# Optimization experiments

Measured on AMD Instinct MI355X. Metric: run time of the kernel, lower is better.

## Reference

```python
import jax, jax.numpy as jnp
import numpy as np

N, E, G, H = 100000, 1600000, 256, 2
EPS = 1e-5


def _gat_conv(x, src, dst, W, a_src, a_dst, bias, C):
    # PyG GATConv (concat=True, negative_slope=0.2): lin has no bias, bias added after concat.
    h = (x @ W).reshape(N, H, C)                                   # [N,H,C]
    e_src = (h * a_src).sum(-1)                                    # [N,H]
    e_dst = (h * a_dst).sum(-1)                                    # [N,H]
    alpha = jax.nn.leaky_relu(e_src[src] + e_dst[dst], 0.2)        # [Etot,H]
    amax = jax.ops.segment_max(alpha, dst, num_segments=N)         # segment softmax over incoming edges
    ex = jnp.exp(alpha - amax[dst])
    denom = jax.ops.segment_sum(ex, dst, num_segments=N)
    msg = h[src] * ex[:, :, None]                                  # [Etot,H,C]
    out = jax.ops.segment_sum(msg, dst, num_segments=N) / (denom[:, :, None] + 1e-16)
    return out.reshape(N, H * C) + bias


def _bn(x, g, b, m, v):  # BatchNorm in eval mode with running stats
    return g * (x - m) * jax.lax.rsqrt(v + EPS) + b


def _forward(edge_index, batch, x, w1, as1, ad1, b1, g1, be1, m1, v1, p1w, p1b,
             w2, as2, ad2, b2, g2, be2, m2, v2, p2w, p2b,
             w3, as3, ad3, b3, g3, be3, m3, v3, p3w, p3b,
             fw, fb, g4, be4, m4, v4, l1w, l1b, l2w, l2b):
    loops = jnp.arange(N, dtype=edge_index.dtype)                  # GATConv add_self_loops=True
    src = jnp.concatenate([edge_index[0], loops])
    dst = jnp.concatenate([edge_index[1], loops])
    h = jax.nn.relu(_bn(_gat_conv(x, src, dst, w1, as1, ad1, b1, 32), g1, be1, m1, v1)) + (x @ p1w + p1b)
    h = jax.nn.relu(_bn(_gat_conv(h, src, dst, w2, as2, ad2, b2, 64), g2, be2, m2, v2)) + (h @ p2w + p2b)
    h = jax.nn.relu(_bn(_gat_conv(h, src, dst, w3, as3, ad3, b3, 64), g3, be3, m3, v3)) + (h @ p3w + p3b)
    counts = jax.ops.segment_sum(jnp.ones((N,), h.dtype), batch, num_segments=G)
    pooled = jax.ops.segment_sum(h, batch, num_segments=G) / jnp.maximum(counts, 1.0)[:, None]  # [G,128]
    z = jax.nn.relu(_bn(pooled @ fw + fb, g4, be4, m4, v4))
    z = jax.nn.relu(z @ l1w + l1b)
    return z @ l2w + l2b                                           # [G,10]


def setup_inputs():
    key = jax.random.key(0)
    ks = jax.random.split(key, 48)
    it = iter(range(48))
    def rn(shape, s=0.1):
        return jax.random.normal(ks[next(it)], shape, jnp.float32) * s
    def bn_params(dim):  # gamma, beta, running_mean, running_var
        return (jax.random.uniform(ks[next(it)], (dim,), jnp.float32, 0.5, 1.5),
                rn((dim,)), rn((dim,)),
                jax.random.uniform(ks[next(it)], (dim,), jnp.float32, 0.5, 1.5))
    inp = {}
    inp["x"] = jax.random.normal(ks[next(it)], (N, 5), jnp.float32)
    inp["edge_index"] = jax.random.randint(ks[next(it)], (2, E), 0, N, jnp.int32)
    inp["batch"] = jnp.sort(jax.random.randint(ks[next(it)], (N,), 0, G, jnp.int32))
    inp["w1"], inp["as1"], inp["ad1"], inp["b1"] = rn((5, 64)), rn((H, 32)), rn((H, 32)), rn((64,))
    inp["g1"], inp["be1"], inp["m1"], inp["v1"] = bn_params(64)
    inp["p1w"], inp["p1b"] = rn((5, 64)), rn((64,))
    inp["w2"], inp["as2"], inp["ad2"], inp["b2"] = rn((64, 128)), rn((H, 64)), rn((H, 64)), rn((128,))
    inp["g2"], inp["be2"], inp["m2"], inp["v2"] = bn_params(128)
    inp["p2w"], inp["p2b"] = rn((64, 128)), rn((128,))
    inp["w3"], inp["as3"], inp["ad3"], inp["b3"] = rn((128, 128)), rn((H, 64)), rn((H, 64)), rn((128,))
    inp["g3"], inp["be3"], inp["m3"], inp["v3"] = bn_params(128)
    inp["p3w"], inp["p3b"] = rn((128, 128)), rn((128,))
    inp["fw"], inp["fb"] = rn((128, 32)), rn((32,))
    inp["g4"], inp["be4"], inp["m4"], inp["v4"] = bn_params(32)
    inp["l1w"], inp["l1b"] = rn((32, 32)), rn((32,))
    inp["l2w"], inp["l2b"] = rn((32, 10)), rn((10,))
    return inp


def reference(x, edge_index, batch, w1, as1, ad1, b1, g1, be1, m1, v1, p1w, p1b,
              w2, as2, ad2, b2, g2, be2, m2, v2, p2w, p2b,
              w3, as3, ad3, b3, g3, be3, m3, v3, p3w, p3b,
              fw, fb, g4, be4, m4, v4, l1w, l1b, l2w, l2b):
    return _forward(edge_index, batch, x, w1, as1, ad1, b1, g1, be1, m1, v1, p1w, p1b,
                    w2, as2, ad2, b2, g2, be2, m2, v2, p2w, p2b,
                    w3, as3, ad3, b3, g3, be3, m3, v3, p3w, p3b,
                    fw, fb, g4, be4, m4, v4, l1w, l1b, l2w, l2b)
```

## Files before the change

kernel.cpp:

```cpp
#include <hip/hip_runtime.h>
#include <hip/hip_bf16.h>
#include <hip/hip_fp16.h>

#define NN   100000
#define EE   1600000
#define ETOT (EE + NN)
#define GG   256
#define BNEPS 1e-5f
#define NBK  391
#define PADTOT (ETOT + NBK * 4096 + 64)
#define PSPLIT 16

typedef float floatx2 __attribute__((ext_vector_type(2)));
typedef short s16x8 __attribute__((ext_vector_type(8)));
typedef float f32x4v __attribute__((ext_vector_type(4)));

__device__ __forceinline__ unsigned short f2bf(float f) {
    unsigned u = __float_as_uint(f);
    unsigned r = u + 0x7FFF + ((u >> 16) & 1);
    return (unsigned short)(r >> 16);
}
__device__ __forceinline__ float bf2f(unsigned short b) {
    return __uint_as_float(((unsigned)b) << 16);
}
__device__ __forceinline__ floatx2 pkfma(floatx2 a, floatx2 b, floatx2 c) {
    return __builtin_elementwise_fma(a, b, c);
}


__global__ __launch_bounds__(256) void bucket_count_kernel(
    const int* __restrict__ ei, int* __restrict__ bucket_cnt)
{
    __shared__ int cnt[NBK];
    for (int i = threadIdx.x; i < NBK; i += 256) cnt[i] = 0;
    __syncthreads();
    int base = blockIdx.x * 8192;
    for (int k = threadIdx.x; k < 8192; k += 256) {
        int e = base + k;
        if (e < ETOT) {
            int dst = (e < EE) ? ei[EE + e] : (e - EE);
            atomicAdd(&cnt[dst >> 8], 1);
        }
    }
    __syncthreads();
    for (int i = threadIdx.x; i < NBK; i += 256)
        if (cnt[i]) atomicAdd(&bucket_cnt[i], cnt[i]);
}

__global__ __launch_bounds__(512) void bucket_scan_kernel(
    const int* __restrict__ bucket_cnt, int* __restrict__ bucket_base,
    int* __restrict__ gcursor, float* __restrict__ esrcs)
{
    __shared__ int s[512];
    int t = threadIdx.x;
    int v = (t < NBK) ? bucket_cnt[t] : 0;
    s[t] = v;
    __syncthreads();
    int x = v;
    for (int o = 1; o < 512; o <<= 1) {
        int y = (t >= o) ? s[t - o] : 0;
        __syncthreads();
        x += y;
        s[t] = x;
        __syncthreads();
    }
    if (t < NBK) { bucket_base[t] = x - v; gcursor[t] = x - v; }
    if (t == 0) {
        bucket_base[NBK] = ETOT;
        esrcs[2 * NN]     = __int_as_float(0xFF800000);
        esrcs[2 * NN + 1] = __int_as_float(0xFF800000);
    }
}

__global__ __launch_bounds__(256) void partition_kernel(
    const int* __restrict__ ei, int* __restrict__ gcursor, int* __restrict__ part)
{
    __shared__ int cnt[NBK];
    __shared__ int basel[NBK];
    for (int i = threadIdx.x; i < NBK; i += 256) cnt[i] = 0;
    __syncthreads();
    int base = blockIdx.x * 4096;
    for (int k = threadIdx.x; k < 4096; k += 256) {
        int e = base + k;
        if (e < ETOT) {
            int dst = (e < EE) ? ei[EE + e] : (e - EE);
            atomicAdd(&cnt[dst >> 8], 1);
        }
    }
    __syncthreads();
    for (int i = threadIdx.x; i < NBK; i += 256) {
        int c = cnt[i];
        basel[i] = c ? atomicAdd(&gcursor[i], c) : 0;
        cnt[i] = 0;
    }
    __syncthreads();
    for (int k = threadIdx.x; k < 4096; k += 256) {
        int e = base + k;
        if (e < ETOT) {
            int src, dst;
            if (e < EE) { src = ei[e]; dst = ei[EE + e]; }
            else        { src = e - EE; dst = e - EE; }
            int b = dst >> 8;
            int slot = atomicAdd(&cnt[b], 1);
            part[basel[b] + slot] = src | ((dst & 255) << 17);
        }
    }
}

__global__ __launch_bounds__(256) void csr_build_kernel(
    const int* __restrict__ part, const int* __restrict__ bucket_base,
    int* __restrict__ row2_start, int* __restrict__ row2_deg,
    int* __restrict__ csr2_src)
{
    __shared__ int degs[256];
    __shared__ int sc[256];
    __shared__ int cur[256];
    int b = blockIdx.x;
    int t = threadIdx.x;
    int beg = bucket_base[b], end = bucket_base[b + 1];
    int pbase = ((beg + 15) & ~15) + 4096 * b;
    degs[t] = 0;
    __syncthreads();
    for (int j = beg + t; j < end; j += 256)
        atomicAdd(&degs[(part[j] >> 17) & 255], 1);
    __syncthreads();
    int dg = degs[t];
    int pdeg = (dg + 15) & ~15;
    sc[t] = pdeg;
    __syncthreads();
    int x = pdeg;
    for (int o = 1; o < 256; o <<= 1) {
        int y = (t >= o) ? sc[t - o] : 0;
        __syncthreads();
        x += y;
        sc[t] = x;
        __syncthreads();
    }
    int start2 = pbase + (x - pdeg);
    int node = b * 256 + t;
    if (node < NN) { row2_start[node] = start2; row2_deg[node] = dg; }
    cur[t] = start2;
    __syncthreads();
    for (int j = beg + t; j < end; j += 256) {
        int pv = part[j];
        int pos = atomicAdd(&cur[(pv >> 17) & 255], 1);
        csr2_src[pos] = pv & 0x1FFFF;
    }
    for (int k = dg; k < pdeg; ++k) csr2_src[start2 + k] = NN;
}


template<int K>
__device__ __forceinline__ void prep_w_body(
    int unit, const float* __restrict__ W, const float* __restrict__ pw,
    short* __restrict__ wfrag)
{
    constexpr int KS = K / 32;
    int total = 16 * KS * 2 * 64;
    if (unit >= total) return;
    int lane = unit & 63;
    int rest = unit >> 6;
    int hilo = rest & 1;
    int fk = rest >> 1;
    int ks = fk % KS;
    int nt = fk / KS;
    int n = nt * 16 + (lane & 15);
    int k0 = ks * 32 + (lane >> 4) * 8;
    const float* src = (n < 128) ? (W + n) : (pw + (n - 128));
    s16x8 out;
#pragma unroll
    for (int j = 0; j < 8; ++j) {
        float wv = src[(size_t)(k0 + j) * 128];
        unsigned short hi = f2bf(wv);
        if (hilo == 0) {
            out[j] = (short)hi;
        } else {
            float fhi = __uint_as_float(((unsigned)hi) << 16);
            out[j] = (short)f2bf(wv - fhi);
        }
    }
    *(s16x8*)(wfrag + (size_t)unit * 8) = out;
}

__global__ __launch_bounds__(256) void prep_all_kernel(
    const float* __restrict__ w2, const float* __restrict__ p2w, short* __restrict__ wfrag2,
    const float* __restrict__ w3, const float* __restrict__ p3w, short* __restrict__ wfrag3,
    const float* b1, const float* g1, const float* be1, const float* m1, const float* v1,
    const float* b2, const float* g2, const float* be2, const float* m2, const float* v2,
    const float* b3, const float* g3, const float* be3, const float* m3, const float* v3,
    float* sc1, float* sh1, float* sc2, float* sh2, float* sc3, float* sh3)
{
    int b = blockIdx.x;
    int tid = threadIdx.x;
    if (b < 16) {
        prep_w_body<64>(b * 256 + tid, w2, p2w, wfrag2);
    } else if (b < 48) {
        prep_w_body<128>((b - 16) * 256 + tid, w3, p3w, wfrag3);
    } else {
        int t = tid;
        if (t < 128) {
            if (t < 64) {
                float sc = g1[t] * rsqrtf(v1[t] + BNEPS);
                sc1[t] = sc;
                sh1[t] = (b1[t] - m1[t]) * sc + be1[t];
            }
            {
                float sc = g2[t] * rsqrtf(v2[t] + BNEPS);
                sc2[t] = sc;
                sh2[t] = (b2[t] - m2[t]) * sc + be2[t];
            }
            {
                float sc = g3[t] * rsqrtf(v3[t] + BNEPS);
                sc3[t] = sc;
                sh3[t] = (b3[t] - m3[t]) * sc + be3[t];
            }
        }
    }
}


__global__ __launch_bounds__(256) void edgew_kernel(
    const int* __restrict__ csr2_src, const int* __restrict__ row2_start,
    const int* __restrict__ row2_deg,
    const float2* __restrict__ esrc, const float2* __restrict__ edst,
    unsigned* __restrict__ csr_w, int nN)
{
    int n = blockIdx.x * 4 + (threadIdx.x >> 6);
    int lane = threadIdx.x & 63;
    if (n >= nN) return;
    float2 ed = edst[n];
    int s2 = row2_start[n];
    int dg = row2_deg[n];
    int pc = (dg + 15) & ~15;
    for (int j = lane; j < pc; j += 64) {
        int i = csr2_src[s2 + j];
        float2 es = esrc[i];
        float a0 = es.x + ed.x; a0 = (a0 > 0.f) ? a0 : 0.2f * a0;
        float a1 = es.y + ed.y; a1 = (a1 > 0.f) ? a1 : 0.2f * a1;
        unsigned w = (unsigned)f2bf(__expf(a0)) | ((unsigned)f2bf(__expf(a1)) << 16);
        csr_w[s2 + j] = w;
    }
}


__global__ __launch_bounds__(256) void feat1_kernel(
    const float* __restrict__ xin, const float* __restrict__ W,
    const float* __restrict__ pw, const float* __restrict__ pb,
    const float* __restrict__ a_src, const float* __restrict__ a_dst,
    unsigned char* __restrict__ h8, float* __restrict__ esrc, float* __restrict__ edst,
    unsigned short* __restrict__ rout16, int nN)
{
    constexpr int F_IN = 5, F_OUT = 64;
    int t = threadIdx.x;
    int n = blockIdx.x * 4 + t / F_OUT;
    int f = t % F_OUT;
    if (n >= nN) return;
    float acc = 0.f, racc = 0.f;
#pragma unroll
    for (int k = 0; k < F_IN; ++k) {
        float xv = xin[n * F_IN + k];
        acc  += xv * W[k * F_OUT + f];
        racc += xv * pw[k * F_OUT + f];
    }
    float other = __shfl_xor(acc, 1, 64);
    if ((f & 1) == 0) {
        int p = __builtin_amdgcn_cvt_pk_fp8_f32(acc, other, 0, false);
        *(unsigned short*)(h8 + (size_t)n * F_OUT + f) = (unsigned short)(p & 0xFFFF);
    }
    rout16[(size_t)n * F_OUT + f] = f2bf(racc + pb[f]);
    float es = acc * a_src[f];
    float ed = acc * a_dst[f];
#pragma unroll
    for (int off = 16; off > 0; off >>= 1) {
        es += __shfl_xor(es, off, 32);
        ed += __shfl_xor(ed, off, 32);
    }
    if ((t & 31) == 0) {
        int head = (f >> 5) & 1;
        esrc[n * 2 + head] = es;
        edst[n * 2 + head] = ed;
    }
}


template<int K>
__global__ __launch_bounds__(256) void mfma_feat_kernel(
    const unsigned short* __restrict__ xin16, const short* __restrict__ wfrag,
    const float* __restrict__ pb,
    const float* __restrict__ a_src, const float* __restrict__ a_dst,
    unsigned char* __restrict__ h8, float* __restrict__ esrc, float* __restrict__ edst,
    unsigned short* __restrict__ rout16)
{
    constexpr int KS = K / 32;
    constexpr int CH = K / 8;
    __shared__ __align__(16) char smem[53248];
    s16x8* xs = (s16x8*)smem;
    unsigned short* h8lds = (unsigned short*)smem;
    unsigned short* rolds = (unsigned short*)(smem + 18432);

    const int tid = threadIdx.x;
    const int base = blockIdx.x * 128;

    for (int idx = tid; idx < 128 * CH; idx += 256) {
        int node = idx / CH;
        int ch = idx % CH;
        int gn = base + node; if (gn > NN - 1) gn = NN - 1;
        s16x8 v = *(const s16x8*)(xin16 + (size_t)gn * K + ch * 8);
        int tt = node >> 4, mm = node & 15;
        xs[(tt * CH + ch) * 16 + mm] = v;
    }
    __syncthreads();

    const int w = tid >> 6;
    const int lane = tid & 63;
    const int quad = lane >> 4;
    const int m = lane & 15;
    const int l0 = w * 32 + quad * 4;
    const int l1 = l0 + 16;
    const int node0 = base + l0;
    const int node1 = base + l1;

    s16x8 a0[KS], a1[KS];
#pragma unroll
    for (int ks = 0; ks < KS; ++ks) {
        a0[ks] = xs[((w * 2 + 0) * CH + (ks * 4 + quad)) * 16 + m];
        a1[ks] = xs[((w * 2 + 1) * CH + (ks * 4 + quad)) * 16 + m];
    }
    __syncthreads();

    float es0h0[4] = {0.f,0.f,0.f,0.f}, es0h1[4] = {0.f,0.f,0.f,0.f};
    float ed0h0[4] = {0.f,0.f,0.f,0.f}, ed0h1[4] = {0.f,0.f,0.f,0.f};
    float es1h0[4] = {0.f,0.f,0.f,0.f}, es1h1[4] = {0.f,0.f,0.f,0.f};
    float ed1h0[4] = {0.f,0.f,0.f,0.f}, ed1h1[4] = {0.f,0.f,0.f,0.f};

#pragma unroll
    for (int nt = 0; nt < 16; ++nt) {
        s16x8 b[2 * KS];
#pragma unroll
        for (int i = 0; i < 2 * KS; ++i)
            b[i] = *(const s16x8*)(wfrag + (size_t)((nt * KS * 2 + i) * 64 + lane) * 8);
        f32x4v c0 = {0.f, 0.f, 0.f, 0.f};
        f32x4v c1 = {0.f, 0.f, 0.f, 0.f};
#pragma unroll
        for (int ks = 0; ks < KS; ++ks) {
            c0 = __builtin_amdgcn_mfma_f32_16x16x32_bf16(a0[ks], b[2 * ks + 0], c0, 0, 0, 0);
            c1 = __builtin_amdgcn_mfma_f32_16x16x32_bf16(a1[ks], b[2 * ks + 0], c1, 0, 0, 0);
            c0 = __builtin_amdgcn_mfma_f32_16x16x32_bf16(a0[ks], b[2 * ks + 1], c0, 0, 0, 0);
            c1 = __builtin_amdgcn_mfma_f32_16x16x32_bf16(a1[ks], b[2 * ks + 1], c1, 0, 0, 0);
        }
        if (nt < 8) {
            int col = nt * 16 + m;
            float av = a_src[col], dv = a_dst[col];
#pragma unroll
            for (int r = 0; r < 4; ++r) {
                float v0 = c0[r], v1 = c1[r];
                if (nt < 4) {
                    es0h0[r] = fmaf(v0, av, es0h0[r]); ed0h0[r] = fmaf(v0, dv, ed0h0[r]);
                    es1h0[r] = fmaf(v1, av, es1h0[r]); ed1h0[r] = fmaf(v1, dv, ed1h0[r]);
                } else {
                    es0h1[r] = fmaf(v0, av, es0h1[r]); ed0h1[r] = fmaf(v0, dv, ed0h1[r]);
                    es1h1[r] = fmaf(v1, av, es1h1[r]); ed1h1[r] = fmaf(v1, dv, ed1h1[r]);
                }
                float p0 = __shfl_xor(v0, 1, 16);
                float p1 = __shfl_xor(v1, 1, 16);
                if ((m & 1) == 0) {
                    int us = nt * 8 + (m >> 1);
                    int pk0 = __builtin_amdgcn_cvt_pk_fp8_f32(v0, p0, 0, false);
                    int pk1 = __builtin_amdgcn_cvt_pk_fp8_f32(v1, p1, 0, false);
                    h8lds[(l0 + r) * 72 + us] = (unsigned short)(pk0 & 0xFFFF);
                    h8lds[(l1 + r) * 72 + us] = (unsigned short)(pk1 & 0xFFFF);
                }
            }
        } else {
            int col = (nt - 8) * 16 + m;
            float bv = pb[col];
#pragma unroll
            for (int r = 0; r < 4; ++r) {
                rolds[(l0 + r) * 136 + col] = f2bf(c0[r] + bv);
                rolds[(l1 + r) * 136 + col] = f2bf(c1[r] + bv);
            }
        }
    }

#pragma unroll
    for (int r = 0; r < 4; ++r) {
#pragma unroll
        for (int off = 8; off > 0; off >>= 1) {
            es0h0[r] += __shfl_xor(es0h0[r], off, 16);
            es0h1[r] += __shfl_xor(es0h1[r], off, 16);
            ed0h0[r] += __shfl_xor(ed0h0[r], off, 16);
            ed0h1[r] += __shfl_xor(ed0h1[r], off, 16);
            es1h0[r] += __shfl_xor(es1h0[r], off, 16);
            es1h1[r] += __shfl_xor(es1h1[r], off, 16);
            ed1h0[r] += __shfl_xor(ed1h0[r], off, 16);
            ed1h1[r] += __shfl_xor(ed1h1[r], off, 16);
        }
    }
    if (m == 0) {
#pragma unroll
        for (int r = 0; r < 4; ++r) {
            if (node0 + r < NN) {
                ((float2*)esrc)[node0 + r] = make_float2(es0h0[r], es0h1[r]);
                ((float2*)edst)[node0 + r] = make_float2(ed0h0[r], ed0h1[r]);
            }
            if (node1 + r < NN) {
                ((float2*)esrc)[node1 + r] = make_float2(es1h0[r], es1h1[r]);
                ((float2*)edst)[node1 + r] = make_float2(ed1h0[r], ed1h1[r]);
            }
        }
    }

    __syncthreads();
    for (int i = tid; i < 128 * 8; i += 256) {
        int row = i >> 3, ch = i & 7;
        int node = base + row;
        if (node < NN) {
            int4 v = *(const int4*)(smem + row * 144 + ch * 16);
            *(int4*)(h8 + (size_t)node * 128 + ch * 16) = v;
        }
    }
    for (int i = tid; i < 128 * 16; i += 256) {
        int row = i >> 4, ch = i & 15;
        int node = base + row;
        if (node < NN) {
            int4 v = *(const int4*)(smem + 18432 + row * 272 + ch * 16);
            *(int4*)((char*)rout16 + (size_t)node * 256 + ch * 16) = v;
        }
    }
}


__global__ __launch_bounds__(256) void aggregate128_kernel(
    const unsigned char* __restrict__ h8,
    const int* __restrict__ row2_start, const int* __restrict__ row2_deg,
    const int* __restrict__ csr2_src, const unsigned* __restrict__ csr_w,
    const float* __restrict__ bnsc, const float* __restrict__ bnsh,
    unsigned short* __restrict__ io16)
{
    int w = threadIdx.x >> 6;
    int lane = threadIdx.x & 63;
    int half = lane >> 5;
    int fl = lane & 31;
    bool headhi = fl >= 16;
    int n = blockIdx.x * 8 + w * 2 + half;
    int s2 = row2_start[n];
    int dg = row2_deg[n];
    int pc = (dg + 15) & ~15;
    const int* sp = csr2_src + s2;
    const unsigned* wp = csr_w + s2;
    float s = 0.f;
    floatx2 acc01 = {0.f, 0.f}, acc23 = {0.f, 0.f};
    for (int j = 0; j < pc; j += 8) {
        int i0 = sp[j + 0];
        int i1 = sp[j + 1];
        int i2 = sp[j + 2];
        int i3 = sp[j + 3];
        int i4 = sp[j + 4];
        int i5 = sp[j + 5];
        int i6 = sp[j + 6];
        int i7 = sp[j + 7];
        unsigned w0 = wp[j + 0];
        unsigned w1 = wp[j + 1];
        unsigned w2 = wp[j + 2];
        unsigned w3 = wp[j + 3];
        unsigned w4 = wp[j + 4];
        unsigned w5 = wp[j + 5];
        unsigned w6 = wp[j + 6];
        unsigned w7 = wp[j + 7];
        unsigned d0 = *(const unsigned*)(h8 + (size_t)i0 * 128 + fl * 4);
        unsigned d1 = *(const unsigned*)(h8 + (size_t)i1 * 128 + fl * 4);
        unsigned d2 = *(const unsigned*)(h8 + (size_t)i2 * 128 + fl * 4);
        unsigned d3 = *(const unsigned*)(h8 + (size_t)i3 * 128 + fl * 4);
        unsigned d4 = *(const unsigned*)(h8 + (size_t)i4 * 128 + fl * 4);
        unsigned d5 = *(const unsigned*)(h8 + (size_t)i5 * 128 + fl * 4);
        unsigned d6 = *(const unsigned*)(h8 + (size_t)i6 * 128 + fl * 4);
        unsigned d7 = *(const unsigned*)(h8 + (size_t)i7 * 128 + fl * 4);
        float g0 = __uint_as_float(headhi ? (w0 & 0xFFFF0000u) : (w0 << 16));
        float g1 = __uint_as_float(headhi ? (w1 & 0xFFFF0000u) : (w1 << 16));
        float g2 = __uint_as_float(headhi ? (w2 & 0xFFFF0000u) : (w2 << 16));
        float g3 = __uint_as_float(headhi ? (w3 & 0xFFFF0000u) : (w3 << 16));
        float g4 = __uint_as_float(headhi ? (w4 & 0xFFFF0000u) : (w4 << 16));
        float g5 = __uint_as_float(headhi ? (w5 & 0xFFFF0000u) : (w5 << 16));
        float g6 = __uint_as_float(headhi ? (w6 & 0xFFFF0000u) : (w6 << 16));
        float g7 = __uint_as_float(headhi ? (w7 & 0xFFFF0000u) : (w7 << 16));
        floatx2 gv0 = {g0, g0};
        floatx2 gv1 = {g1, g1};
        floatx2 gv2 = {g2, g2};
        floatx2 gv3 = {g3, g3};
        floatx2 gv4 = {g4, g4};
        floatx2 gv5 = {g5, g5};
        floatx2 gv6 = {g6, g6};
        floatx2 gv7 = {g7, g7};
        acc01 = pkfma(gv0, __builtin_amdgcn_cvt_pk_f32_fp8((int)d0, false), acc01);
        acc23 = pkfma(gv0, __builtin_amdgcn_cvt_pk_f32_fp8((int)d0, true),  acc23);
        acc01 = pkfma(gv1, __builtin_amdgcn_cvt_pk_f32_fp8((int)d1, false), acc01);
        acc23 = pkfma(gv1, __builtin_amdgcn_cvt_pk_f32_fp8((int)d1, true),  acc23);
        acc01 = pkfma(gv2, __builtin_amdgcn_cvt_pk_f32_fp8((int)d2, false), acc01);
        acc23 = pkfma(gv2, __builtin_amdgcn_cvt_pk_f32_fp8((int)d2, true),  acc23);
        acc01 = pkfma(gv3, __builtin_amdgcn_cvt_pk_f32_fp8((int)d3, false), acc01);
        acc23 = pkfma(gv3, __builtin_amdgcn_cvt_pk_f32_fp8((int)d3, true),  acc23);
        acc01 = pkfma(gv4, __builtin_amdgcn_cvt_pk_f32_fp8((int)d4, false), acc01);
        acc23 = pkfma(gv4, __builtin_amdgcn_cvt_pk_f32_fp8((int)d4, true),  acc23);
        acc01 = pkfma(gv5, __builtin_amdgcn_cvt_pk_f32_fp8((int)d5, false), acc01);
        acc23 = pkfma(gv5, __builtin_amdgcn_cvt_pk_f32_fp8((int)d5, true),  acc23);
        acc01 = pkfma(gv6, __builtin_amdgcn_cvt_pk_f32_fp8((int)d6, false), acc01);
        acc23 = pkfma(gv6, __builtin_amdgcn_cvt_pk_f32_fp8((int)d6, true),  acc23);
        acc01 = pkfma(gv7, __builtin_amdgcn_cvt_pk_f32_fp8((int)d7, false), acc01);
        acc23 = pkfma(gv7, __builtin_amdgcn_cvt_pk_f32_fp8((int)d7, true),  acc23);
        s += (((g0 + g1) + (g2 + g3)) + ((g4 + g5) + (g6 + g7)));
    }
    float inv = 1.f / (s + 1e-16f);
    int f0 = fl * 4;
    float4 sc = *(const float4*)(bnsc + f0);
    float4 sh = *(const float4*)(bnsh + f0);
    float o0 = fmaf(acc01.x * inv, sc.x, sh.x);
    float o1 = fmaf(acc01.y * inv, sc.y, sh.y);
    float o2 = fmaf(acc23.x * inv, sc.z, sh.z);
    float o3 = fmaf(acc23.y * inv, sc.w, sh.w);
    uint2* iop = (uint2*)(io16 + (size_t)n * 128 + f0);
    uint2 pu = *iop;
    float r0 = fmaxf(o0, 0.f) + __uint_as_float((pu.x & 0xFFFFu) << 16);
    float r1 = fmaxf(o1, 0.f) + __uint_as_float(pu.x & 0xFFFF0000u);
    float r2 = fmaxf(o2, 0.f) + __uint_as_float((pu.y & 0xFFFFu) << 16);
    float r3 = fmaxf(o3, 0.f) + __uint_as_float(pu.y & 0xFFFF0000u);
    uint2 ov;
    ov.x = (unsigned)f2bf(r0) | ((unsigned)f2bf(r1) << 16);
    ov.y = (unsigned)f2bf(r2) | ((unsigned)f2bf(r3) << 16);
    *iop = ov;
}


__global__ __launch_bounds__(256) void aggregate64_kernel(
    const unsigned char* __restrict__ h8,
    const int* __restrict__ row2_start, const int* __restrict__ row2_deg,
    const int* __restrict__ csr2_src, const unsigned* __restrict__ csr_w,
    const float* __restrict__ bnsc, const float* __restrict__ bnsh,
    unsigned short* __restrict__ io16)
{
    int w = threadIdx.x >> 6;
    int lane = threadIdx.x & 63;
    int half = lane >> 5;
    int hl = lane & 31;
    int q  = hl >> 4;
    int fl = hl & 15;
    bool headhi = (fl >> 3) & 1;
    int n = blockIdx.x * 8 + w * 2 + half;
    int s2 = row2_start[n];
    int dg = row2_deg[n];
    int pc = (dg + 15) & ~15;
    const int4* sp = (const int4*)(csr2_src + s2);
    const uint4* wp = (const uint4*)(csr_w + s2);
    float s = 0.f;
    floatx2 acc01 = {0.f, 0.f}, acc23 = {0.f, 0.f};
    for (int j = 0; j < pc; j += 8) {
        int4 ia = sp[(j >> 2) + 0];
        int4 ib = sp[(j >> 2) + 1];
        uint4 wa = wp[(j >> 2) + 0];
        uint4 wb = wp[(j >> 2) + 1];
        int i0 = q ? ia.y : ia.x;
        int i1 = q ? ia.w : ia.z;
        int i2 = q ? ib.y : ib.x;
        int i3 = q ? ib.w : ib.z;
        unsigned w0 = q ? wa.y : wa.x;
        unsigned w1 = q ? wa.w : wa.z;
        unsigned w2 = q ? wb.y : wb.x;
        unsigned w3 = q ? wb.w : wb.z;
        unsigned d0 = *(const unsigned*)(h8 + (size_t)i0 * 64 + fl * 4);
        unsigned d1 = *(const unsigned*)(h8 + (size_t)i1 * 64 + fl * 4);
        unsigned d2 = *(const unsigned*)(h8 + (size_t)i2 * 64 + fl * 4);
        unsigned d3 = *(const unsigned*)(h8 + (size_t)i3 * 64 + fl * 4);
        float g0 = __uint_as_float(headhi ? (w0 & 0xFFFF0000u) : (w0 << 16));
        float g1 = __uint_as_float(headhi ? (w1 & 0xFFFF0000u) : (w1 << 16));
        float g2 = __uint_as_float(headhi ? (w2 & 0xFFFF0000u) : (w2 << 16));
        float g3 = __uint_as_float(headhi ? (w3 & 0xFFFF0000u) : (w3 << 16));
        floatx2 gv0 = {g0, g0};
        floatx2 gv1 = {g1, g1};
        floatx2 gv2 = {g2, g2};
        floatx2 gv3 = {g3, g3};
        acc01 = pkfma(gv0, __builtin_amdgcn_cvt_pk_f32_fp8((int)d0, false), acc01);
        acc23 = pkfma(gv0, __builtin_amdgcn_cvt_pk_f32_fp8((int)d0, true),  acc23);
        acc01 = pkfma(gv1, __builtin_amdgcn_cvt_pk_f32_fp8((int)d1, false), acc01);
        acc23 = pkfma(gv1, __builtin_amdgcn_cvt_pk_f32_fp8((int)d1, true),  acc23);
        acc01 = pkfma(gv2, __builtin_amdgcn_cvt_pk_f32_fp8((int)d2, false), acc01);
        acc23 = pkfma(gv2, __builtin_amdgcn_cvt_pk_f32_fp8((int)d2, true),  acc23);
        acc01 = pkfma(gv3, __builtin_amdgcn_cvt_pk_f32_fp8((int)d3, false), acc01);
        acc23 = pkfma(gv3, __builtin_amdgcn_cvt_pk_f32_fp8((int)d3, true),  acc23);
        s += ((g0 + g1) + (g2 + g3));
    }
    acc01.x += __shfl_xor(acc01.x, 16);
    acc01.y += __shfl_xor(acc01.y, 16);
    acc23.x += __shfl_xor(acc23.x, 16);
    acc23.y += __shfl_xor(acc23.y, 16);
    s += __shfl_xor(s, 16);
    if (hl < 16) {
        float inv = 1.f / (s + 1e-16f);
        int f0 = fl * 4;
        float4 sc = *(const float4*)(bnsc + f0);
        float4 sh = *(const float4*)(bnsh + f0);
        float o0 = fmaf(acc01.x * inv, sc.x, sh.x);
        float o1 = fmaf(acc01.y * inv, sc.y, sh.y);
        float o2 = fmaf(acc23.x * inv, sc.z, sh.z);
        float o3 = fmaf(acc23.y * inv, sc.w, sh.w);
        uint2* iop = (uint2*)(io16 + (size_t)n * 64 + f0);
        uint2 pu = *iop;
        float r0 = fmaxf(o0, 0.f) + __uint_as_float((pu.x & 0xFFFFu) << 16);
        float r1 = fmaxf(o1, 0.f) + __uint_as_float(pu.x & 0xFFFF0000u);
        float r2 = fmaxf(o2, 0.f) + __uint_as_float((pu.y & 0xFFFFu) << 16);
        float r3 = fmaxf(o3, 0.f) + __uint_as_float(pu.y & 0xFFFF0000u);
        uint2 ov;
        ov.x = (unsigned)f2bf(r0) | ((unsigned)f2bf(r1) << 16);
        ov.y = (unsigned)f2bf(r2) | ((unsigned)f2bf(r3) << 16);
        *iop = ov;
    }
}


__global__ __launch_bounds__(128) void pool_partial_kernel(
    const unsigned short* __restrict__ hf16, const int* __restrict__ batch,
    float* __restrict__ ppart)
{
    int g = blockIdx.x / PSPLIT;
    int p = blockIdx.x % PSPLIT;
    int f = threadIdx.x;
    int lo = 0, hi = NN;
    while (lo < hi) { int mid = (lo + hi) >> 1; if (batch[mid] < g) lo = mid + 1; else hi = mid; }
    int start = lo;
    hi = NN;
    while (lo < hi) { int mid = (lo + hi) >> 1; if (batch[mid] < g + 1) lo = mid + 1; else hi = mid; }
    int end = lo;
    int len = end - start;
    int chunk = (len + PSPLIT - 1) / PSPLIT;
    int i0 = start + p * chunk;
    int i1 = i0 + chunk; if (i1 > end) i1 = end;
    float acc = 0.f;
    for (int i = i0; i < i1; ++i) acc += bf2f(hf16[(size_t)i * 128 + f]);
    ppart[((size_t)g * PSPLIT + p) * 128 + f] = acc;
}


__global__ __launch_bounds__(128) void head_kernel(
    const float* __restrict__ ppart, const int* __restrict__ batch,
    const float* __restrict__ fw, const float* __restrict__ fb,
    const float* __restrict__ g4, const float* __restrict__ be4,
    const float* __restrict__ m4, const float* __restrict__ v4,
    const float* __restrict__ l1w, const float* __restrict__ l1b,
    const float* __restrict__ l2w, const float* __restrict__ l2b,
    float* __restrict__ out)
{
    __shared__ float p[128];
    __shared__ float z1[32];
    __shared__ float z2[32];
    int g = blockIdx.x, t = threadIdx.x;
    int lo = 0, hi = NN;
    while (lo < hi) { int mid = (lo + hi) >> 1; if (batch[mid] < g) lo = mid + 1; else hi = mid; }
    int start = lo;
    hi = NN;
    while (lo < hi) { int mid = (lo + hi) >> 1; if (batch[mid] < g + 1) lo = mid + 1; else hi = mid; }
    float cnt = (float)(lo - start);
    float acc = 0.f;
#pragma unroll
    for (int q = 0; q < PSPLIT; ++q)
        acc += ppart[((size_t)g * PSPLIT + q) * 128 + t];
    p[t] = acc / fmaxf(cnt, 1.0f);
    __syncthreads();
    if (t < 32) {
        float a = fb[t];
        for (int k = 0; k < 128; ++k) a += p[k] * fw[k * 32 + t];
        float val = g4[t] * (a - m4[t]) * rsqrtf(v4[t] + BNEPS) + be4[t];
        z1[t] = fmaxf(val, 0.f);
    }
    __syncthreads();
    if (t < 32) {
        float a = l1b[t];
        for (int k = 0; k < 32; ++k) a += z1[k] * l1w[k * 32 + t];
        z2[t] = fmaxf(a, 0.f);
    }
    __syncthreads();
    if (t < 10) {
        float a = l2b[t];
        for (int k = 0; k < 32; ++k) a += z2[k] * l2w[k * 10 + t];
        out[g * 10 + t] = a;
    }
}


extern "C" void kernel_launch(void* const* d_in, const int* in_sizes, int n_in,
                              void* d_out, int out_size, void* d_ws, size_t ws_size,
                              hipStream_t stream) {
    const float* x     = (const float*)d_in[0];
    const int*   ei    = (const int*)d_in[1];
    const int*   batch = (const int*)d_in[2];
    const float* w1  = (const float*)d_in[3];
    const float* as1 = (const float*)d_in[4];
    const float* ad1 = (const float*)d_in[5];
    const float* b1  = (const float*)d_in[6];
    const float* g1  = (const float*)d_in[7];
    const float* be1 = (const float*)d_in[8];
    const float* m1  = (const float*)d_in[9];
    const float* v1  = (const float*)d_in[10];
    const float* p1w = (const float*)d_in[11];
    const float* p1b = (const float*)d_in[12];
    const float* w2  = (const float*)d_in[13];
    const float* as2 = (const float*)d_in[14];
    const float* ad2 = (const float*)d_in[15];
    const float* b2  = (const float*)d_in[16];
    const float* g2  = (const float*)d_in[17];
    const float* be2 = (const float*)d_in[18];
    const float* m2  = (const float*)d_in[19];
    const float* v2  = (const float*)d_in[20];
    const float* p2w = (const float*)d_in[21];
    const float* p2b = (const float*)d_in[22];
    const float* w3  = (const float*)d_in[23];
    const float* as3 = (const float*)d_in[24];
    const float* ad3 = (const float*)d_in[25];
    const float* b3  = (const float*)d_in[26];
    const float* g3  = (const float*)d_in[27];
    const float* be3 = (const float*)d_in[28];
    const float* m3  = (const float*)d_in[29];
    const float* v3  = (const float*)d_in[30];
    const float* p3w = (const float*)d_in[31];
    const float* p3b = (const float*)d_in[32];
    const float* fw  = (const float*)d_in[33];
    const float* fb  = (const float*)d_in[34];
    const float* g4  = (const float*)d_in[35];
    const float* be4 = (const float*)d_in[36];
    const float* m4  = (const float*)d_in[37];
    const float* v4  = (const float*)d_in[38];
    const float* l1w = (const float*)d_in[39];
    const float* l1b = (const float*)d_in[40];
    const float* l2w = (const float*)d_in[41];
    const float* l2b = (const float*)d_in[42];

    char* ws = (char*)d_ws;
    size_t off = 0;
    auto alloc = [&](size_t bytes) -> char* {
        char* p = ws + off;
        off += (bytes + 255) & ~(size_t)255;
        return p;
    };
    int*    bucket_cnt  = (int*)alloc((NBK) * sizeof(int));
    int*    bucket_base = (int*)alloc((NBK + 1) * sizeof(int));
    int*    gcursor     = (int*)alloc((NBK) * sizeof(int));
    int*    part        = (int*)alloc((size_t)ETOT * sizeof(int));
    int*    row2_start  = (int*)alloc(NN * sizeof(int));
    int*    row2_deg    = (int*)alloc(NN * sizeof(int));
    int*    csr2_src    = (int*)alloc((size_t)PADTOT * sizeof(int));
    unsigned* csr_w     = (unsigned*)alloc((size_t)PADTOT * sizeof(unsigned));
    unsigned char*  h8  = (unsigned char*)alloc((size_t)(NN + 1) * 128);
    unsigned short* hb1 = (unsigned short*)alloc((size_t)NN * 64 * sizeof(short));
    unsigned short* hb2 = (unsigned short*)alloc((size_t)NN * 128 * sizeof(short));
    unsigned short* hb3 = (unsigned short*)alloc((size_t)NN * 128 * sizeof(short));
    float*  esrc        = (float*)alloc((size_t)(NN + 1) * 2 * sizeof(float));
    float*  edst        = (float*)alloc((size_t)NN * 2 * sizeof(float));
    float*  ppart       = (float*)alloc((size_t)GG * PSPLIT * 128 * sizeof(float));
    short*  wfrag2      = (short*)alloc((size_t)16 * 2 * 2 * 64 * 8 * sizeof(short));
    short*  wfrag3      = (short*)alloc((size_t)16 * 4 * 2 * 64 * 8 * sizeof(short));
    float*  bnsc1       = (float*)alloc(64 * sizeof(float));
    float*  bnsh1       = (float*)alloc(64 * sizeof(float));
    float*  bnsc2       = (float*)alloc(128 * sizeof(float));
    float*  bnsh2       = (float*)alloc(128 * sizeof(float));
    float*  bnsc3       = (float*)alloc(128 * sizeof(float));
    float*  bnsh3       = (float*)alloc(128 * sizeof(float));

    prep_all_kernel<<<49, 256, 0, stream>>>(
        w2, p2w, wfrag2, w3, p3w, wfrag3,
        b1, g1, be1, m1, v1, b2, g2, be2, m2, v2, b3, g3, be3, m3, v3,
        bnsc1, bnsh1, bnsc2, bnsh2, bnsc3, bnsh3);

    hipMemsetAsync(bucket_cnt, 0, NBK * sizeof(int), stream);
    bucket_count_kernel<<<(ETOT + 8191) / 8192, 256, 0, stream>>>(ei, bucket_cnt);
    bucket_scan_kernel<<<1, 512, 0, stream>>>(bucket_cnt, bucket_base, gcursor, esrc);
    partition_kernel<<<(ETOT + 4095) / 4096, 256, 0, stream>>>(ei, gcursor, part);
    csr_build_kernel<<<NBK, 256, 0, stream>>>(part, bucket_base, row2_start, row2_deg, csr2_src);

    feat1_kernel<<<(NN + 3) / 4, 256, 0, stream>>>(
        x, w1, p1w, p1b, as1, ad1, h8, esrc, edst, hb1, NN);
    edgew_kernel<<<(NN + 3) / 4, 256, 0, stream>>>(
        csr2_src, row2_start, row2_deg, (const float2*)esrc, (const float2*)edst, csr_w, NN);
    aggregate64_kernel<<<NN / 8, 256, 0, stream>>>(
        h8, row2_start, row2_deg, csr2_src, csr_w, bnsc1, bnsh1, hb1);

    mfma_feat_kernel<64><<<(NN + 127) / 128, 256, 0, stream>>>(
        hb1, wfrag2, p2b, as2, ad2, h8, esrc, edst, hb2);
    edgew_kernel<<<(NN + 3) / 4, 256, 0, stream>>>(
        csr2_src, row2_start, row2_deg, (const float2*)esrc, (const float2*)edst, csr_w, NN);
    aggregate128_kernel<<<NN / 8, 256, 0, stream>>>(
        h8, row2_start, row2_deg, csr2_src, csr_w, bnsc2, bnsh2, hb2);

    mfma_feat_kernel<128><<<(NN + 127) / 128, 256, 0, stream>>>(
        hb2, wfrag3, p3b, as3, ad3, h8, esrc, edst, hb3);
    edgew_kernel<<<(NN + 3) / 4, 256, 0, stream>>>(
        csr2_src, row2_start, row2_deg, (const float2*)esrc, (const float2*)edst, csr_w, NN);
    aggregate128_kernel<<<NN / 8, 256, 0, stream>>>(
        h8, row2_start, row2_deg, csr2_src, csr_w, bnsc3, bnsh3, hb3);

    pool_partial_kernel<<<GG * PSPLIT, 128, 0, stream>>>(hb3, batch, ppart);
    head_kernel<<<GG, 128, 0, stream>>>(ppart, batch, fw, fb, g4, be4, m4, v4,
                                        l1w, l1b, l2w, l2b, (float*)d_out);
}
```

Baseline: 525.2 us.

## Assign one wavefront per node in GAT aggregation, splitting edges across lanes

The aggregation kernels now map one 64-lane wavefront to each destination node instead of two nodes per wave. The lanes split the edge list (2 edge groups for 128 features, 4 for 64) and combine partial sums with cross-lane shuffles. Node index, row start and degree are made wave-uniform with readfirstlane, and the head-select branch becomes a shift. This doubles the grid and gives more independent gather loads per node to hide latency, at the cost of extra shuffle reductions and idle lanes during the epilogue.

Result: slower. 539.1 us (+2.6%).

```diff
diff --git a/kernel.cpp b/kernel.cpp
--- a/kernel.cpp
+++ b/kernel.cpp
@@ -437,116 +437,13 @@
     const float* __restrict__ bnsc, const float* __restrict__ bnsh,
     unsigned short* __restrict__ io16)
 {
-    int w = threadIdx.x >> 6;
     int lane = threadIdx.x & 63;
-    int half = lane >> 5;
+    int e2 = lane >> 5;
     int fl = lane & 31;
-    bool headhi = fl >= 16;
-    int n = blockIdx.x * 8 + w * 2 + half;
-    int s2 = row2_start[n];
-    int dg = row2_deg[n];
-    int pc = (dg + 15) & ~15;
-    const int* sp = csr2_src + s2;
-    const unsigned* wp = csr_w + s2;
-    float s = 0.f;
-    floatx2 acc01 = {0.f, 0.f}, acc23 = {0.f, 0.f};
-    for (int j = 0; j < pc; j += 8) {
-        int i0 = sp[j + 0];
-        int i1 = sp[j + 1];
-        int i2 = sp[j + 2];
-        int i3 = sp[j + 3];
-        int i4 = sp[j + 4];
-        int i5 = sp[j + 5];
-        int i6 = sp[j + 6];
-        int i7 = sp[j + 7];
-        unsigned w0 = wp[j + 0];
-        unsigned w1 = wp[j + 1];
-        unsigned w2 = wp[j + 2];
-        unsigned w3 = wp[j + 3];
-        unsigned w4 = wp[j + 4];
-        unsigned w5 = wp[j + 5];
-        unsigned w6 = wp[j + 6];
-        unsigned w7 = wp[j + 7];
-        unsigned d0 = *(const unsigned*)(h8 + (size_t)i0 * 128 + fl * 4);
-        unsigned d1 = *(const unsigned*)(h8 + (size_t)i1 * 128 + fl * 4);
-        unsigned d2 = *(const unsigned*)(h8 + (size_t)i2 * 128 + fl * 4);
-        unsigned d3 = *(const unsigned*)(h8 + (size_t)i3 * 128 + fl * 4);
-        unsigned d4 = *(const unsigned*)(h8 + (size_t)i4 * 128 + fl * 4);
-        unsigned d5 = *(const unsigned*)(h8 + (size_t)i5 * 128 + fl * 4);
-        unsigned d6 = *(const unsigned*)(h8 + (size_t)i6 * 128 + fl * 4);
-        unsigned d7 = *(const unsigned*)(h8 + (size_t)i7 * 128 + fl * 4);
-        float g0 = __uint_as_float(headhi ? (w0 & 0xFFFF0000u) : (w0 << 16));
-        float g1 = __uint_as_float(headhi ? (w1 & 0xFFFF0000u) : (w1 << 16));
-        float g2 = __uint_as_float(headhi ? (w2 & 0xFFFF0000u) : (w2 << 16));
-        float g3 = __uint_as_float(headhi ? (w3 & 0xFFFF0000u) : (w3 << 16));
-        float g4 = __uint_as_float(headhi ? (w4 & 0xFFFF0000u) : (w4 << 16));
-        float g5 = __uint_as_float(headhi ? (w5 & 0xFFFF0000u) : (w5 << 16));
-        float g6 = __uint_as_float(headhi ? (w6 & 0xFFFF0000u) : (w6 << 16));
-        float g7 = __uint_as_float(headhi ? (w7 & 0xFFFF0000u) : (w7 << 16));
-        floatx2 gv0 = {g0, g0};
-        floatx2 gv1 = {g1, g1};
-        floatx2 gv2 = {g2, g2};
-        floatx2 gv3 = {g3, g3};
-        floatx2 gv4 = {g4, g4};
-        floatx2 gv5 = {g5, g5};
-        floatx2 gv6 = {g6, g6};
-        floatx2 gv7 = {g7, g7};
-        acc01 = pkfma(gv0, __builtin_amdgcn_cvt_pk_f32_fp8((int)d0, false), acc01);
-        acc23 = pkfma(gv0, __builtin_amdgcn_cvt_pk_f32_fp8((int)d0, true),  acc23);
-        acc01 = pkfma(gv1, __builtin_amdgcn_cvt_pk_f32_fp8((int)d1, false), acc01);
-        acc23 = pkfma(gv1, __builtin_amdgcn_cvt_pk_f32_fp8((int)d1, true),  acc23);
-        acc01 = pkfma(gv2, __builtin_amdgcn_cvt_pk_f32_fp8((int)d2, false), acc01);
-        acc23 = pkfma(gv2, __builtin_amdgcn_cvt_pk_f32_fp8((int)d2, true),  acc23);
-        acc01 = pkfma(gv3, __builtin_amdgcn_cvt_pk_f32_fp8((int)d3, false), acc01);
-        acc23 = pkfma(gv3, __builtin_amdgcn_cvt_pk_f32_fp8((int)d3, true),  acc23);
-        acc01 = pkfma(gv4, __builtin_amdgcn_cvt_pk_f32_fp8((int)d4, false), acc01);
-        acc23 = pkfma(gv4, __builtin_amdgcn_cvt_pk_f32_fp8((int)d4, true),  acc23);
-        acc01 = pkfma(gv5, __builtin_amdgcn_cvt_pk_f32_fp8((int)d5, false), acc01);
-        acc23 = pkfma(gv5, __builtin_amdgcn_cvt_pk_f32_fp8((int)d5, true),  acc23);
-        acc01 = pkfma(gv6, __builtin_amdgcn_cvt_pk_f32_fp8((int)d6, false), acc01);
-        acc23 = pkfma(gv6, __builtin_amdgcn_cvt_pk_f32_fp8((int)d6, true),  acc23);
-        acc01 = pkfma(gv7, __builtin_amdgcn_cvt_pk_f32_fp8((int)d7, false), acc01);
-        acc23 = pkfma(gv7, __builtin_amdgcn_cvt_pk_f32_fp8((int)d7, true),  acc23);
-        s += (((g0 + g1) + (g2 + g3)) + ((g4 + g5) + (g6 + g7)));
-    }
-    float inv = 1.f / (s + 1e-16f);
-    int f0 = fl * 4;
-    float4 sc = *(const float4*)(bnsc + f0);
-    float4 sh = *(const float4*)(bnsh + f0);
-    float o0 = fmaf(acc01.x * inv, sc.x, sh.x);
-    float o1 = fmaf(acc01.y * inv, sc.y, sh.y);
-    float o2 = fmaf(acc23.x * inv, sc.z, sh.z);
-    float o3 = fmaf(acc23.y * inv, sc.w, sh.w);
-    uint2* iop = (uint2*)(io16 + (size_t)n * 128 + f0);
-    uint2 pu = *iop;
-    float r0 = fmaxf(o0, 0.f) + __uint_as_float((pu.x & 0xFFFFu) << 16);
-    float r1 = fmaxf(o1, 0.f) + __uint_as_float(pu.x & 0xFFFF0000u);
-    float r2 = fmaxf(o2, 0.f) + __uint_as_float((pu.y & 0xFFFFu) << 16);
-    float r3 = fmaxf(o3, 0.f) + __uint_as_float(pu.y & 0xFFFF0000u);
-    uint2 ov;
-    ov.x = (unsigned)f2bf(r0) | ((unsigned)f2bf(r1) << 16);
-    ov.y = (unsigned)f2bf(r2) | ((unsigned)f2bf(r3) << 16);
-    *iop = ov;
-}
-
-
-__global__ __launch_bounds__(256) void aggregate64_kernel(
-    const unsigned char* __restrict__ h8,
-    const int* __restrict__ row2_start, const int* __restrict__ row2_deg,
-    const int* __restrict__ csr2_src, const unsigned* __restrict__ csr_w,
-    const float* __restrict__ bnsc, const float* __restrict__ bnsh,
-    unsigned short* __restrict__ io16)
-{
-    int w = threadIdx.x >> 6;
-    int lane = threadIdx.x & 63;
-    int half = lane >> 5;
-    int hl = lane & 31;
-    int q  = hl >> 4;
-    int fl = hl & 15;
-    bool headhi = (fl >> 3) & 1;
-    int n = blockIdx.x * 8 + w * 2 + half;
-    int s2 = row2_start[n];
-    int dg = row2_deg[n];
+    unsigned shl = (fl >= 16) ? 0u : 16u;
+    int n = __builtin_amdgcn_readfirstlane(blockIdx.x * 4 + (threadIdx.x >> 6));
+    int s2 = __builtin_amdgcn_readfirstlane(row2_start[n]);
+    int dg = __builtin_amdgcn_readfirstlane(row2_deg[n]);
     int pc = (dg + 15) & ~15;
     const int4* sp = (const int4*)(csr2_src + s2);
     const uint4* wp = (const uint4*)(csr_w + s2);
@@ -557,22 +454,22 @@
         int4 ib = sp[(j >> 2) + 1];
         uint4 wa = wp[(j >> 2) + 0];
         uint4 wb = wp[(j >> 2) + 1];
-        int i0 = q ? ia.y : ia.x;
-        int i1 = q ? ia.w : ia.z;
-        int i2 = q ? ib.y : ib.x;
-        int i3 = q ? ib.w : ib.z;
-        unsigned w0 = q ? wa.y : wa.x;
-        unsigned w1 = q ? wa.w : wa.z;
-        unsigned w2 = q ? wb.y : wb.x;
-        unsigned w3 = q ? wb.w : wb.z;
-        unsigned d0 = *(const unsigned*)(h8 + (size_t)i0 * 64 + fl * 4);
-        unsigned d1 = *(const unsigned*)(h8 + (size_t)i1 * 64 + fl * 4);
-        unsigned d2 = *(const unsigned*)(h8 + (size_t)i2 * 64 + fl * 4);
-        unsigned d3 = *(const unsigned*)(h8 + (size_t)i3 * 64 + fl * 4);
-        float g0 = __uint_as_float(headhi ? (w0 & 0xFFFF0000u) : (w0 << 16));
-        float g1 = __uint_as_float(headhi ? (w1 & 0xFFFF0000u) : (w1 << 16));
-        float g2 = __uint_as_float(headhi ? (w2 & 0xFFFF0000u) : (w2 << 16));
-        float g3 = __uint_as_float(headhi ? (w3 & 0xFFFF0000u) : (w3 << 16));
+        int i0 = e2 ? ia.y : ia.x;
+        int i1 = e2 ? ia.w : ia.z;
+        int i2 = e2 ? ib.y : ib.x;
+        int i3 = e2 ? ib.w : ib.z;
+        unsigned w0 = e2 ? wa.y : wa.x;
+        unsigned w1 = e2 ? wa.w : wa.z;
+        unsigned w2 = e2 ? wb.y : wb.x;
+        unsigned w3 = e2 ? wb.w : wb.z;
+        unsigned d0 = *(const unsigned*)(h8 + (size_t)i0 * 128 + fl * 4);
+        unsigned d1 = *(const unsigned*)(h8 + (size_t)i1 * 128 + fl * 4);
+        unsigned d2 = *(const unsigned*)(h8 + (size_t)i2 * 128 + fl * 4);
+        unsigned d3 = *(const unsigned*)(h8 + (size_t)i3 * 128 + fl * 4);
+        float g0 = __uint_as_float((w0 << shl) & 0xFFFF0000u);
+        float g1 = __uint_as_float((w1 << shl) & 0xFFFF0000u);
+        float g2 = __uint_as_float((w2 << shl) & 0xFFFF0000u);
+        float g3 = __uint_as_float((w3 << shl) & 0xFFFF0000u);
         floatx2 gv0 = {g0, g0};
         floatx2 gv1 = {g1, g1};
         floatx2 gv2 = {g2, g2};
@@ -587,12 +484,93 @@
         acc23 = pkfma(gv3, __builtin_amdgcn_cvt_pk_f32_fp8((int)d3, true),  acc23);
         s += ((g0 + g1) + (g2 + g3));
     }
+    acc01.x += __shfl_xor(acc01.x, 32);
+    acc01.y += __shfl_xor(acc01.y, 32);
+    acc23.x += __shfl_xor(acc23.x, 32);
+    acc23.y += __shfl_xor(acc23.y, 32);
+    s += __shfl_xor(s, 32);
+    if (e2 == 0) {
+        float inv = 1.f / (s + 1e-16f);
+        int f0 = fl * 4;
+        float4 sc = *(const float4*)(bnsc + f0);
+        float4 sh = *(const float4*)(bnsh + f0);
+        float o0 = fmaf(acc01.x * inv, sc.x, sh.x);
+        float o1 = fmaf(acc01.y * inv, sc.y, sh.y);
+        float o2 = fmaf(acc23.x * inv, sc.z, sh.z);
+        float o3 = fmaf(acc23.y * inv, sc.w, sh.w);
+        uint2* iop = (uint2*)(io16 + (size_t)n * 128 + f0);
+        uint2 pu = *iop;
+        float r0 = fmaxf(o0, 0.f) + __uint_as_float((pu.x & 0xFFFFu) << 16);
+        float r1 = fmaxf(o1, 0.f) + __uint_as_float(pu.x & 0xFFFF0000u);
+        float r2 = fmaxf(o2, 0.f) + __uint_as_float((pu.y & 0xFFFFu) << 16);
+        float r3 = fmaxf(o3, 0.f) + __uint_as_float(pu.y & 0xFFFF0000u);
+        uint2 ov;
+        ov.x = (unsigned)f2bf(r0) | ((unsigned)f2bf(r1) << 16);
+        ov.y = (unsigned)f2bf(r2) | ((unsigned)f2bf(r3) << 16);
+        *iop = ov;
+    }
+}
+
+
+__global__ __launch_bounds__(256) void aggregate64_kernel(
+    const unsigned char* __restrict__ h8,
+    const int* __restrict__ row2_start, const int* __restrict__ row2_deg,
+    const int* __restrict__ csr2_src, const unsigned* __restrict__ csr_w,
+    const float* __restrict__ bnsc, const float* __restrict__ bnsh,
+    unsigned short* __restrict__ io16)
+{
+    int lane = threadIdx.x & 63;
+    int e4 = lane >> 4;
+    int fl = lane & 15;
+    unsigned shl = (fl >= 8) ? 0u : 16u;
+    int n = __builtin_amdgcn_readfirstlane(blockIdx.x * 4 + (threadIdx.x >> 6));
+    int s2 = __builtin_amdgcn_readfirstlane(row2_start[n]);
+    int dg = __builtin_amdgcn_readfirstlane(row2_deg[n]);
+    int pc = (dg + 15) & ~15;
+    const int4* sp = (const int4*)(csr2_src + s2);
+    const uint4* wp = (const uint4*)(csr_w + s2);
+    float s = 0.f;
+    floatx2 acc01 = {0.f, 0.f}, acc23 = {0.f, 0.f};
+    for (int j = 0; j < pc; j += 8) {
+        int4 ia = sp[(j >> 2) + 0];
+        int4 ib = sp[(j >> 2) + 1];
+        uint4 wa = wp[(j >> 2) + 0];
+        uint4 wb = wp[(j >> 2) + 1];
+        int ta0 = (e4 & 1) ? ia.y : ia.x;
+        int tb0 = (e4 & 1) ? ia.w : ia.z;
+        int i0  = (e4 & 2) ? tb0 : ta0;
+        int ta1 = (e4 & 1) ? ib.y : ib.x;
+        int tb1 = (e4 & 1) ? ib.w : ib.z;
+        int i1  = (e4 & 2) ? tb1 : ta1;
+        unsigned ua0 = (e4 & 1) ? wa.y : wa.x;
+        unsigned ub0 = (e4 & 1) ? wa.w : wa.z;
+        unsigned w0  = (e4 & 2) ? ub0 : ua0;
+        unsigned ua1 = (e4 & 1) ? wb.y : wb.x;
+        unsigned ub1 = (e4 & 1) ? wb.w : wb.z;
+        unsigned w1  = (e4 & 2) ? ub1 : ua1;
+        unsigned d0 = *(const unsigned*)(h8 + (size_t)i0 * 64 + fl * 4);
+        unsigned d1 = *(const unsigned*)(h8 + (size_t)i1 * 64 + fl * 4);
+        float g0 = __uint_as_float((w0 << shl) & 0xFFFF0000u);
+        float g1 = __uint_as_float((w1 << shl) & 0xFFFF0000u);
+        floatx2 gv0 = {g0, g0};
+        floatx2 gv1 = {g1, g1};
+        acc01 = pkfma(gv0, __builtin_amdgcn_cvt_pk_f32_fp8((int)d0, false), acc01);
+        acc23 = pkfma(gv0, __builtin_amdgcn_cvt_pk_f32_fp8((int)d0, true),  acc23);
+        acc01 = pkfma(gv1, __builtin_amdgcn_cvt_pk_f32_fp8((int)d1, false), acc01);
+        acc23 = pkfma(gv1, __builtin_amdgcn_cvt_pk_f32_fp8((int)d1, true),  acc23);
+        s += (g0 + g1);
+    }
     acc01.x += __shfl_xor(acc01.x, 16);
     acc01.y += __shfl_xor(acc01.y, 16);
     acc23.x += __shfl_xor(acc23.x, 16);
     acc23.y += __shfl_xor(acc23.y, 16);
     s += __shfl_xor(s, 16);
-    if (hl < 16) {
+    acc01.x += __shfl_xor(acc01.x, 32);
+    acc01.y += __shfl_xor(acc01.y, 32);
+    acc23.x += __shfl_xor(acc23.x, 32);
+    acc23.y += __shfl_xor(acc23.y, 32);
+    s += __shfl_xor(s, 32);
+    if (e4 == 0) {
         float inv = 1.f / (s + 1e-16f);
         int f0 = fl * 4;
         float4 sc = *(const float4*)(bnsc + f0);
@@ -777,21 +755,21 @@
         x, w1, p1w, p1b, as1, ad1, h8, esrc, edst, hb1, NN);
     edgew_kernel<<<(NN + 3) / 4, 256, 0, stream>>>(
         csr2_src, row2_start, row2_deg, (const float2*)esrc, (const float2*)edst, csr_w, NN);
-    aggregate64_kernel<<<NN / 8, 256, 0, stream>>>(
+    aggregate64_kernel<<<NN / 4, 256, 0, stream>>>(
         h8, row2_start, row2_deg, csr2_src, csr_w, bnsc1, bnsh1, hb1);
 
     mfma_feat_kernel<64><<<(NN + 127) / 128, 256, 0, stream>>>(
         hb1, wfrag2, p2b, as2, ad2, h8, esrc, edst, hb2);
     edgew_kernel<<<(NN + 3) / 4, 256, 0, stream>>>(
         csr2_src, row2_start, row2_deg, (const float2*)esrc, (const float2*)edst, csr_w, NN);
-    aggregate128_kernel<<<NN / 8, 256, 0, stream>>>(
+    aggregate128_kernel<<<NN / 4, 256, 0, stream>>>(
         h8, row2_start, row2_deg, csr2_src, csr_w, bnsc2, bnsh2, hb2);
 
     mfma_feat_kernel<128><<<(NN + 127) / 128, 256, 0, stream>>>(
         hb2, wfrag3, p3b, as3, ad3, h8, esrc, edst, hb3);
     edgew_kernel<<<(NN + 3) / 4, 256, 0, stream>>>(
         csr2_src, row2_start, row2_deg, (const float2*)esrc, (const float2*)edst, csr_w, NN);
-    aggregate128_kernel<<<NN / 8, 256, 0, stream>>>(
+    aggregate128_kernel<<<NN / 4, 256, 0, stream>>>(
         h8, row2_start, row2_deg, csr2_src, csr_w, bnsc3, bnsh3, hb3);
 
     pool_partial_kernel<<<GG * PSPLIT, 128, 0, stream>>>(hb3, batch, ppart);
```
